# Kernel tuning notes

Hardware: AMD Instinct MI355X
Metric: run time of the kernel (lower is better)

The kernel has to match this reference:

```python
import jax, jax.numpy as jnp
import numpy as np


def _knn_idx(pts, k):
    # pts: [N, d] -> indices of k nearest neighbors (incl. self, loop=True) [N, k]
    sq = jnp.sum(pts * pts, axis=-1)
    d2 = sq[:, None] + sq[None, :] - 2.0 * (pts @ pts.T)  # [N, N] squared dists
    _, idx = jax.lax.top_k(-d2, k)  # k smallest distances
    return idx


def _graph_conv(x, nbr, Wr, br, Ws):
    # x: [B, N, d_in], nbr: [B, N, k]. GraphConv (aggr='add'):
    # out_i = W_rel @ sum_j x_j + b_rel + W_root @ x_i
    gathered = jax.vmap(lambda xb, ib: xb[ib])(x, nbr)  # [B, N, k, d_in]
    agg = gathered.sum(axis=2)                          # [B, N, d_in]
    return agg @ Wr.T + br + x @ Ws.T


def setup_inputs() -> dict:
    key = jax.random.key(0)
    ks = jax.random.split(key, 10)
    B, N, D, H = 16, 2048, 3, 128
    s = lambda fi, fo: (2.0 / (fi + fo)) ** 0.5
    return {
        "point_cloud": jax.random.normal(ks[0], (B, N, D), dtype=jnp.float32),
        "W1r": jax.random.normal(ks[1], (H, D), dtype=jnp.float32) * s(D, H),
        "b1": jnp.zeros((H,), dtype=jnp.float32),
        "W1s": jax.random.normal(ks[2], (H, D), dtype=jnp.float32) * s(D, H),
        "W2r": jax.random.normal(ks[3], (H, H), dtype=jnp.float32) * s(H, H),
        "b2": jnp.zeros((H,), dtype=jnp.float32),
        "W2s": jax.random.normal(ks[4], (H, H), dtype=jnp.float32) * s(H, H),
        "W3r": jax.random.normal(ks[5], (H, H), dtype=jnp.float32) * s(H, H),
        "b3": jnp.zeros((H,), dtype=jnp.float32),
        "W3s": jax.random.normal(ks[6], (H, H), dtype=jnp.float32) * s(H, H),
        "k": 16,
    }


def reference(point_cloud, W1r, b1, W1s, W2r, b2, W2s, W3r, b3, W3s, k):
    # knn graph per batch element (loop=True: self-loop included, d(i,i)=0)
    nbr = jax.vmap(lambda p: _knn_idx(p, k))(point_cloud)  # [B, N, k]
    x = jax.nn.relu(_graph_conv(point_cloud, nbr, W1r, b1, W1s))
    x = jax.nn.relu(_graph_conv(x, nbr, W2r, b2, W2s))
    x = _graph_conv(x, nbr, W3r, b3, W3s)
    return x  # [B, N, output_dim]
```

## Files before the change

### kernel.cpp

```cpp
#include <hip/hip_runtime.h>
#include <math.h>

#define NPTS 2048
#define BATCH 16
#define KNN 16
#define HID 128
#define RPB 8
#define CAP 128

typedef __attribute__((ext_vector_type(8))) short bf16x8;
typedef __attribute__((ext_vector_type(4))) float f32x4;

__device__ inline unsigned short f2bf(float f) {
    unsigned u = __float_as_uint(f);
    return (unsigned short)((u + 0x7FFFu + ((u >> 16) & 1u)) >> 16);
}
__device__ inline float bflo(unsigned v) { return __uint_as_float(v << 16); }
__device__ inline float bfhi(unsigned v) { return __uint_as_float(v & 0xFFFF0000u); }

__global__ __launch_bounds__(512) void knn_kernel(const float* __restrict__ pc,
                                                  int* __restrict__ nbr,
                                                  float4* __restrict__ aggpc)
{
    __shared__ __align__(16) float4 pts[NPTS];
    __shared__ unsigned ckey[RPB][CAP];
    __shared__ unsigned cidx[RPB][CAP];

    const int b = blockIdx.x >> 8;
    const int rblk = blockIdx.x & 255;
    const float* p = pc + (size_t)b * NPTS * 3;

    for (int t = threadIdx.x; t < NPTS; t += 512) {
        float x = p[t * 3 + 0], y = p[t * 3 + 1], z = p[t * 3 + 2];
        pts[t] = make_float4(x, y, z, x * x + y * y + z * z);
    }
    __syncthreads();

    const int w = threadIdx.x >> 6;
    const int lane = threadIdx.x & 63;
    const int i = rblk * RPB + w;
    const float4 pi = pts[i];

    unsigned key[32];
    #pragma unroll
    for (int t = 0; t < 32; ++t) {
        float4 c = pts[t * 64 + lane];
        float dot = fmaf(pi.x, c.x, fmaf(pi.y, c.y, pi.z * c.z));
        float d2 = fmaf(-2.0f, dot, pi.w + c.w);
        key[t] = __float_as_uint(d2 + 16.0f);
    }

    unsigned km = 0xFFFFFFFFu;
    #pragma unroll
    for (int t = 0; t < 32; ++t) km = min(km, key[t]);

    unsigned v = km;
    #pragma unroll
    for (int k = 2; k <= 64; k <<= 1) {
        #pragma unroll
        for (int j = k >> 1; j > 0; j >>= 1) {
            unsigned o = (unsigned)__shfl_xor((int)v, j, 64);
            bool up = ((lane & k) == 0);
            bool lower = ((lane & j) == 0);
            unsigned mn = min(v, o), mx = max(v, o);
            v = (up == lower) ? mn : mx;
        }
    }
    const unsigned T0 = (unsigned)__shfl((int)v, 15, 64);

    unsigned base = 0;
    #pragma unroll 1
    for (int t = 0; t < 32; ++t) {
        bool pred = key[t] <= T0;
        unsigned long long mask = __ballot(pred);
        if (mask) {
            unsigned prefix = __builtin_amdgcn_mbcnt_hi(
                (unsigned)(mask >> 32),
                __builtin_amdgcn_mbcnt_lo((unsigned)mask, 0));
            unsigned pos = base + prefix;
            if (pred && pos < CAP) {
                ckey[w][pos] = key[t];
                cidx[w][pos] = (unsigned)(t * 64 + lane);
            }
            base += (unsigned)__popcll(mask);
        }
    }
    __threadfence_block();
    const int m = (int)base;

    int* out = nbr + ((size_t)b * NPTS + i) * KNN;
    float ax = 0.f, ay = 0.f, az = 0.f;

    if (m <= CAP) {
        unsigned k0 = (lane < m) ? ckey[w][lane] : 0xFFFFFFFFu;
        unsigned k1 = (lane + 64 < m) ? ckey[w][lane + 64] : 0xFFFFFFFFu;
        int r0 = 0, r1 = 0;
        if (m <= 64) {
            #pragma unroll 1
            for (int jj = 0; jj < m; ++jj) {
                unsigned kj = ckey[w][jj];
                r0 += (kj < k0) || (kj == k0 && jj < lane);
            }
        } else {
            #pragma unroll 1
            for (int jj = 0; jj < m; ++jj) {
                unsigned kj = ckey[w][jj];
                r0 += (kj < k0) || (kj == k0 && jj < lane);
                r1 += (kj < k1) || (kj == k1 && jj < lane + 64);
            }
        }
        if (lane < m && r0 < KNN) {
            unsigned j = cidx[w][lane];
            out[r0] = (int)j;
            float4 q = pts[j]; ax += q.x; ay += q.y; az += q.z;
        }
        if (m > 64 && lane + 64 < m && r1 < KNN) {
            unsigned j = cidx[w][lane + 64];
            out[r1] = (int)j;
            float4 q = pts[j]; ax += q.x; ay += q.y; az += q.z;
        }
    } else {
        unsigned T = 0;
        #pragma unroll 1
        for (int bit = 31; bit >= 0; --bit) {
            unsigned trial = T | (1u << bit);
            int cnt = 0;
            #pragma unroll
            for (int t = 0; t < 32; ++t) cnt += (key[t] < trial);
            #pragma unroll
            for (int off = 32; off; off >>= 1)
                cnt += __shfl_xor(cnt, off, 64);
            if (cnt < KNN) T = trial;
        }
        unsigned bs = 0;
        #pragma unroll 1
        for (int t = 0; t < 32; ++t) {
            bool p1 = key[t] < T;
            unsigned long long mask = __ballot(p1);
            if (mask) {
                unsigned prefix = __builtin_amdgcn_mbcnt_hi(
                    (unsigned)(mask >> 32),
                    __builtin_amdgcn_mbcnt_lo((unsigned)mask, 0));
                if (p1) {
                    out[bs + prefix] = t * 64 + lane;
                    float4 q = pts[t * 64 + lane];
                    ax += q.x; ay += q.y; az += q.z;
                }
                bs += (unsigned)__popcll(mask);
            }
        }
        #pragma unroll 1
        for (int t = 0; t < 32 && bs < KNN; ++t) {
            bool p2 = key[t] == T;
            unsigned long long mask = __ballot(p2);
            if (mask) {
                unsigned prefix = __builtin_amdgcn_mbcnt_hi(
                    (unsigned)(mask >> 32),
                    __builtin_amdgcn_mbcnt_lo((unsigned)mask, 0));
                unsigned pos = bs + prefix;
                if (p2 && pos < KNN) {
                    out[pos] = t * 64 + lane;
                    float4 q = pts[t * 64 + lane];
                    ax += q.x; ay += q.y; az += q.z;
                }
                bs += (unsigned)__popcll(mask);
            }
        }
    }

    #pragma unroll
    for (int off = 32; off; off >>= 1) {
        ax += __shfl_xor(ax, off, 64);
        ay += __shfl_xor(ay, off, 64);
        az += __shfl_xor(az, off, 64);
    }
    if (lane == 0)
        aggpc[(size_t)b * NPTS + i] = make_float4(ax, ay, az, 0.f);
}

__global__ __launch_bounds__(256) void layer1_kernel(
    const float* __restrict__ pc, const float4* __restrict__ aggpc,
    const float* __restrict__ W1r, const float* __restrict__ b1,
    const float* __restrict__ W1s, unsigned short* __restrict__ x1)
{
    int gid = blockIdx.x * 256 + threadIdx.x;
    int p = gid >> 7;
    int h = gid & 127;
    float4 a = aggpc[p];
    float xx = pc[(size_t)p * 3 + 0];
    float xy = pc[(size_t)p * 3 + 1];
    float xz = pc[(size_t)p * 3 + 2];
    float acc = b1[h];
    acc += W1r[h * 3 + 0] * a.x + W1r[h * 3 + 1] * a.y + W1r[h * 3 + 2] * a.z;
    acc += W1s[h * 3 + 0] * xx + W1s[h * 3 + 1] * xy + W1s[h * 3 + 2] * xz;
    x1[gid] = f2bf(fmaxf(acc, 0.f));
}

__global__ __launch_bounds__(256) void wcvt_kernel(
    const float* __restrict__ a, const float* __restrict__ b,
    const float* __restrict__ c, const float* __restrict__ d,
    unsigned short* __restrict__ out)
{
    int g = blockIdx.x * 256 + threadIdx.x;
    int m = g >> 14;
    const float* s = (m == 0) ? a : (m == 1) ? b : (m == 2) ? c : d;
    out[g] = f2bf(s[g & 16383]);
}

template <bool RELU, bool OUT_BF16>
__global__ __launch_bounds__(512) void conv_fused(
    const unsigned short* __restrict__ x, const int* __restrict__ nbr,
    const unsigned short* __restrict__ Wr, const unsigned short* __restrict__ Ws,
    const float* __restrict__ bias, void* __restrict__ outv)
{
    __shared__ __align__(16) unsigned short aggs[64][136];
    __shared__ int nbrs[64][17];
    const int p0 = blockIdx.x * 64;
    const int bt = p0 >> 11;
    const unsigned short* xb = x + ((size_t)bt << 11) * HID;

    for (int e = threadIdx.x; e < 64 * KNN; e += 512)
        nbrs[e >> 4][e & 15] = nbr[(size_t)p0 * KNN + e];
    __syncthreads();

    #pragma unroll
    for (int it = 0; it < 2; ++it) {
        int task = it * 512 + threadIdx.x;
        int c8 = task & 15, pt = task >> 4;
        const unsigned short* base = xb + c8 * 8;
        float s[8] = {0, 0, 0, 0, 0, 0, 0, 0};
        #pragma unroll
        for (int t = 0; t < KNN; ++t) {
            int j = nbrs[pt][t];
            uint4 v = *(const uint4*)(base + (size_t)j * HID);
            s[0] += bflo(v.x); s[1] += bfhi(v.x);
            s[2] += bflo(v.y); s[3] += bfhi(v.y);
            s[4] += bflo(v.z); s[5] += bfhi(v.z);
            s[6] += bflo(v.w); s[7] += bfhi(v.w);
        }
        uint4 ov;
        ov.x = (unsigned)f2bf(s[0]) | ((unsigned)f2bf(s[1]) << 16);
        ov.y = (unsigned)f2bf(s[2]) | ((unsigned)f2bf(s[3]) << 16);
        ov.z = (unsigned)f2bf(s[4]) | ((unsigned)f2bf(s[5]) << 16);
        ov.w = (unsigned)f2bf(s[6]) | ((unsigned)f2bf(s[7]) << 16);
        *(uint4*)&aggs[pt][c8 * 8] = ov;
    }
    __syncthreads();

    const int wv = threadIdx.x >> 6;
    const int lane = threadIdx.x & 63;
    const int ptw = (wv & 1) * 32;
    const int h0w = (wv >> 1) * 32;
    const int row = lane & 15;
    const int quad = lane >> 4;

    f32x4 acc[2][2];
    #pragma unroll
    for (int i = 0; i < 2; ++i)
        #pragma unroll
        for (int n = 0; n < 2; ++n) acc[i][n] = (f32x4){0, 0, 0, 0};

    #pragma unroll
    for (int kc = 0; kc < 4; ++kc) {
        bf16x8 a0 = *(const bf16x8*)&aggs[ptw + row][quad * 8 + kc * 32];
        bf16x8 a1 = *(const bf16x8*)&aggs[ptw + 16 + row][quad * 8 + kc * 32];
        #pragma unroll
        for (int n = 0; n < 2; ++n) {
            bf16x8 bb = *(const bf16x8*)&Wr[(size_t)(h0w + n * 16 + row) * HID
                                            + quad * 8 + kc * 32];
            acc[0][n] = __builtin_amdgcn_mfma_f32_16x16x32_bf16(a0, bb, acc[0][n], 0, 0, 0);
            acc[1][n] = __builtin_amdgcn_mfma_f32_16x16x32_bf16(a1, bb, acc[1][n], 0, 0, 0);
        }
    }
    const unsigned short* xr0 = x + (size_t)(p0 + ptw + row) * HID + quad * 8;
    const unsigned short* xr1 = xr0 + 16 * HID;
    #pragma unroll
    for (int kc = 0; kc < 4; ++kc) {
        bf16x8 a0 = *(const bf16x8*)(xr0 + kc * 32);
        bf16x8 a1 = *(const bf16x8*)(xr1 + kc * 32);
        #pragma unroll
        for (int n = 0; n < 2; ++n) {
            bf16x8 bb = *(const bf16x8*)&Ws[(size_t)(h0w + n * 16 + row) * HID
                                            + quad * 8 + kc * 32];
            acc[0][n] = __builtin_amdgcn_mfma_f32_16x16x32_bf16(a0, bb, acc[0][n], 0, 0, 0);
            acc[1][n] = __builtin_amdgcn_mfma_f32_16x16x32_bf16(a1, bb, acc[1][n], 0, 0, 0);
        }
    }

    #pragma unroll
    for (int n = 0; n < 2; ++n) {
        float bh = bias[h0w + n * 16 + row];
        #pragma unroll
        for (int i = 0; i < 2; ++i) {
            #pragma unroll
            for (int r = 0; r < 4; ++r) {
                int pp = p0 + ptw + i * 16 + quad * 4 + r;
                float vv = acc[i][n][r] + bh;
                if (RELU) vv = fmaxf(vv, 0.f);
                if (OUT_BF16)
                    ((unsigned short*)outv)[(size_t)pp * HID + h0w + n * 16 + row] = f2bf(vv);
                else
                    ((float*)outv)[(size_t)pp * HID + h0w + n * 16 + row] = vv;
            }
        }
    }
}

extern "C" void kernel_launch(void* const* d_in, const int* in_sizes, int n_in,
                              void* d_out, int out_size, void* d_ws, size_t ws_size,
                              hipStream_t stream)
{
    const float* pc  = (const float*)d_in[0];
    const float* W1r = (const float*)d_in[1];
    const float* b1  = (const float*)d_in[2];
    const float* W1s = (const float*)d_in[3];
    const float* W2r = (const float*)d_in[4];
    const float* b2  = (const float*)d_in[5];
    const float* W2s = (const float*)d_in[6];
    const float* W3r = (const float*)d_in[7];
    const float* b3  = (const float*)d_in[8];
    const float* W3s = (const float*)d_in[9];
    float* out = (float*)d_out;

    char* ws = (char*)d_ws;
    const size_t MB = 1024 * 1024;
    int*            nbr   = (int*)ws;
    float4*         aggpc = (float4*)(ws + 2 * MB);
    unsigned short* x1    = (unsigned short*)(ws + 3 * MB);
    unsigned short* x2    = (unsigned short*)(ws + 3 * MB + 8388608);
    unsigned short* wbf   = (unsigned short*)(ws + 3 * MB + 2 * 8388608);
    unsigned short* w2r = wbf;
    unsigned short* w2s = wbf + 16384;
    unsigned short* w3r = wbf + 32768;
    unsigned short* w3s = wbf + 49152;

    const int NPOINTS = BATCH * NPTS;

    knn_kernel<<<NPOINTS / RPB, 512, 0, stream>>>(pc, nbr, aggpc);
    layer1_kernel<<<NPOINTS * HID / 256, 256, 0, stream>>>(
        pc, aggpc, W1r, b1, W1s, x1);
    wcvt_kernel<<<256, 256, 0, stream>>>(W2r, W2s, W3r, W3s, wbf);

    conv_fused<true, true><<<NPOINTS / 64, 512, 0, stream>>>(
        x1, nbr, w2r, w2s, b2, x2);
    conv_fused<false, false><<<NPOINTS / 64, 512, 0, stream>>>(
        x2, nbr, w3r, w3s, b3, out);
}
```

Measured before the change: 184.7 us.

## Fuse layer-1 GraphConv into KNN kernel and use LDS atomics for candidate compaction

Folds the first GraphConv layer into the KNN kernel, so each wavefront writes its bf16 128-wide output row directly and the aggpc buffer and a separate kernel launch go away. Candidate collection switches from ballot/mbcnt prefix compaction to per-wave LDS atomicAdd, storing key and index together as uint2. Ties are now broken by index rather than by slot position, since atomic ordering is nondeterministic. The wcvt launch moves ahead of KNN. The trade-offs are possible LDS atomic contention and a heavier KNN epilogue.

```diff
diff --git a/kernel.cpp b/kernel.cpp
--- a/kernel.cpp
+++ b/kernel.cpp
@@ -18,13 +18,14 @@
 __device__ inline float bflo(unsigned v) { return __uint_as_float(v << 16); }
 __device__ inline float bfhi(unsigned v) { return __uint_as_float(v & 0xFFFF0000u); }
 
-__global__ __launch_bounds__(512) void knn_kernel(const float* __restrict__ pc,
-                                                  int* __restrict__ nbr,
-                                                  float4* __restrict__ aggpc)
+__global__ __launch_bounds__(512) void knn_kernel(
+    const float* __restrict__ pc, int* __restrict__ nbr,
+    const float* __restrict__ W1r, const float* __restrict__ b1,
+    const float* __restrict__ W1s, unsigned short* __restrict__ x1)
 {
     __shared__ __align__(16) float4 pts[NPTS];
-    __shared__ unsigned ckey[RPB][CAP];
-    __shared__ unsigned cidx[RPB][CAP];
+    __shared__ uint2 cand[RPB][CAP];
+    __shared__ unsigned ccnt[RPB];
 
     const int b = blockIdx.x >> 8;
     const int rblk = blockIdx.x & 255;
@@ -40,19 +41,21 @@
     const int lane = threadIdx.x & 63;
     const int i = rblk * RPB + w;
     const float4 pi = pts[i];
+    const float piw16 = pi.w + 16.0f;
+
+    if (lane == 0) ccnt[w] = 0;
+    __threadfence_block();
 
     unsigned key[32];
+    unsigned km = 0xFFFFFFFFu;
     #pragma unroll
     for (int t = 0; t < 32; ++t) {
         float4 c = pts[t * 64 + lane];
         float dot = fmaf(pi.x, c.x, fmaf(pi.y, c.y, pi.z * c.z));
-        float d2 = fmaf(-2.0f, dot, pi.w + c.w);
-        key[t] = __float_as_uint(d2 + 16.0f);
-    }
-
-    unsigned km = 0xFFFFFFFFu;
-    #pragma unroll
-    for (int t = 0; t < 32; ++t) km = min(km, key[t]);
+        float d2 = fmaf(-2.0f, dot, piw16 + c.w);
+        key[t] = __float_as_uint(d2);
+        km = min(km, key[t]);
+    }
 
     unsigned v = km;
     #pragma unroll
@@ -60,64 +63,53 @@
         #pragma unroll
         for (int j = k >> 1; j > 0; j >>= 1) {
             unsigned o = (unsigned)__shfl_xor((int)v, j, 64);
-            bool up = ((lane & k) == 0);
-            bool lower = ((lane & j) == 0);
-            unsigned mn = min(v, o), mx = max(v, o);
-            v = (up == lower) ? mn : mx;
+            bool sel = ((lane & k) == 0) == ((lane & j) == 0);
+            v = sel ? min(v, o) : max(v, o);
         }
     }
     const unsigned T0 = (unsigned)__shfl((int)v, 15, 64);
 
-    unsigned base = 0;
     #pragma unroll 1
     for (int t = 0; t < 32; ++t) {
-        bool pred = key[t] <= T0;
-        unsigned long long mask = __ballot(pred);
-        if (mask) {
-            unsigned prefix = __builtin_amdgcn_mbcnt_hi(
-                (unsigned)(mask >> 32),
-                __builtin_amdgcn_mbcnt_lo((unsigned)mask, 0));
-            unsigned pos = base + prefix;
-            if (pred && pos < CAP) {
-                ckey[w][pos] = key[t];
-                cidx[w][pos] = (unsigned)(t * 64 + lane);
-            }
-            base += (unsigned)__popcll(mask);
+        if (key[t] <= T0) {
+            unsigned pos = atomicAdd(&ccnt[w], 1u);
+            if (pos < CAP)
+                cand[w][pos] = make_uint2(key[t], (unsigned)(t * 64 + lane));
         }
     }
     __threadfence_block();
-    const int m = (int)base;
+    const int m = (int)ccnt[w];
 
     int* out = nbr + ((size_t)b * NPTS + i) * KNN;
     float ax = 0.f, ay = 0.f, az = 0.f;
 
     if (m <= CAP) {
-        unsigned k0 = (lane < m) ? ckey[w][lane] : 0xFFFFFFFFu;
-        unsigned k1 = (lane + 64 < m) ? ckey[w][lane + 64] : 0xFFFFFFFFu;
-        int r0 = 0, r1 = 0;
+        uint2 e0 = (lane < m) ? cand[w][lane] : make_uint2(0xFFFFFFFFu, 0xFFFFFFFFu);
+        int r0 = 0;
         if (m <= 64) {
             #pragma unroll 1
             for (int jj = 0; jj < m; ++jj) {
-                unsigned kj = ckey[w][jj];
-                r0 += (kj < k0) || (kj == k0 && jj < lane);
+                uint2 cj = cand[w][jj];
+                r0 += (cj.x < e0.x) || (cj.x == e0.x && cj.y < e0.y);
             }
         } else {
+            uint2 e1 = (lane + 64 < m) ? cand[w][lane + 64]
+                                       : make_uint2(0xFFFFFFFFu, 0xFFFFFFFFu);
+            int r1 = 0;
             #pragma unroll 1
             for (int jj = 0; jj < m; ++jj) {
-                unsigned kj = ckey[w][jj];
-                r0 += (kj < k0) || (kj == k0 && jj < lane);
-                r1 += (kj < k1) || (kj == k1 && jj < lane + 64);
+                uint2 cj = cand[w][jj];
+                r0 += (cj.x < e0.x) || (cj.x == e0.x && cj.y < e0.y);
+                r1 += (cj.x < e1.x) || (cj.x == e1.x && cj.y < e1.y);
+            }
+            if (lane + 64 < m && r1 < KNN) {
+                out[r1] = (int)e1.y;
+                float4 q = pts[e1.y]; ax += q.x; ay += q.y; az += q.z;
             }
         }
         if (lane < m && r0 < KNN) {
-            unsigned j = cidx[w][lane];
-            out[r0] = (int)j;
-            float4 q = pts[j]; ax += q.x; ay += q.y; az += q.z;
-        }
-        if (m > 64 && lane + 64 < m && r1 < KNN) {
-            unsigned j = cidx[w][lane + 64];
-            out[r1] = (int)j;
-            float4 q = pts[j]; ax += q.x; ay += q.y; az += q.z;
+            out[r0] = (int)e0.y;
+            float4 q = pts[e0.y]; ax += q.x; ay += q.y; az += q.z;
         }
     } else {
         unsigned T = 0;
@@ -174,26 +166,16 @@
         ay += __shfl_xor(ay, off, 64);
         az += __shfl_xor(az, off, 64);
     }
-    if (lane == 0)
-        aggpc[(size_t)b * NPTS + i] = make_float4(ax, ay, az, 0.f);
-}
-
-__global__ __launch_bounds__(256) void layer1_kernel(
-    const float* __restrict__ pc, const float4* __restrict__ aggpc,
-    const float* __restrict__ W1r, const float* __restrict__ b1,
-    const float* __restrict__ W1s, unsigned short* __restrict__ x1)
-{
-    int gid = blockIdx.x * 256 + threadIdx.x;
-    int p = gid >> 7;
-    int h = gid & 127;
-    float4 a = aggpc[p];
-    float xx = pc[(size_t)p * 3 + 0];
-    float xy = pc[(size_t)p * 3 + 1];
-    float xz = pc[(size_t)p * 3 + 2];
-    float acc = b1[h];
-    acc += W1r[h * 3 + 0] * a.x + W1r[h * 3 + 1] * a.y + W1r[h * 3 + 2] * a.z;
-    acc += W1s[h * 3 + 0] * xx + W1s[h * 3 + 1] * xy + W1s[h * 3 + 2] * xz;
-    x1[gid] = f2bf(fmaxf(acc, 0.f));
+
+    unsigned short* xrow = x1 + ((size_t)b * NPTS + i) * HID;
+    #pragma unroll
+    for (int hh = 0; hh < 2; ++hh) {
+        int h = lane + hh * 64;
+        float acc = b1[h];
+        acc += W1r[h * 3 + 0] * ax + W1r[h * 3 + 1] * ay + W1r[h * 3 + 2] * az;
+        acc += W1s[h * 3 + 0] * pi.x + W1s[h * 3 + 1] * pi.y + W1s[h * 3 + 2] * pi.z;
+        xrow[h] = f2bf(fmaxf(acc, 0.f));
+    }
 }
 
 __global__ __launch_bounds__(256) void wcvt_kernel(
@@ -324,11 +306,10 @@
 
     char* ws = (char*)d_ws;
     const size_t MB = 1024 * 1024;
-    int*            nbr   = (int*)ws;
-    float4*         aggpc = (float4*)(ws + 2 * MB);
-    unsigned short* x1    = (unsigned short*)(ws + 3 * MB);
-    unsigned short* x2    = (unsigned short*)(ws + 3 * MB + 8388608);
-    unsigned short* wbf   = (unsigned short*)(ws + 3 * MB + 2 * 8388608);
+    int*            nbr = (int*)ws;
+    unsigned short* x1  = (unsigned short*)(ws + 2 * MB);
+    unsigned short* x2  = (unsigned short*)(ws + 2 * MB + 8388608);
+    unsigned short* wbf = (unsigned short*)(ws + 2 * MB + 2 * 8388608);
     unsigned short* w2r = wbf;
     unsigned short* w2s = wbf + 16384;
     unsigned short* w3r = wbf + 32768;
@@ -336,10 +317,8 @@
 
     const int NPOINTS = BATCH * NPTS;
 
-    knn_kernel<<<NPOINTS / RPB, 512, 0, stream>>>(pc, nbr, aggpc);
-    layer1_kernel<<<NPOINTS * HID / 256, 256, 0, stream>>>(
-        pc, aggpc, W1r, b1, W1s, x1);
     wcvt_kernel<<<256, 256, 0, stream>>>(W2r, W2s, W3r, W3s, wbf);
+    knn_kernel<<<NPOINTS / RPB, 512, 0, stream>>>(pc, nbr, W1r, b1, W1s, x1);
 
     conv_fused<true, true><<<NPOINTS / 64, 512, 0, stream>>>(
         x1, nbr, w2r, w2s, b2, x2);
```

New measurement: 196.8 us. +6.6%, slower.

## Fuse layer-1 conv into kNN epilogue and widen conv blocks to 1024 threads

Applied to the files above, without the earlier changes.

The first GraphConv layer is computed directly in the kNN kernel's epilogue from the wave-reduced neighbor sum. This removes the separate layer1 launch and the aggpc intermediate buffer. The fused conv kernel now uses 1024 threads, with one gather task per thread and 16x32 MFMA tiles per wave instead of 32x32, for more parallelism in the gather phase. The kNN distance loop also folds the bias constant and the min reduction into one pass. The stricter launch bound may limit registers and reduce per-wave reuse of weight loads.

```diff
diff --git a/kernel.cpp b/kernel.cpp
--- a/kernel.cpp
+++ b/kernel.cpp
@@ -18,9 +18,10 @@
 __device__ inline float bflo(unsigned v) { return __uint_as_float(v << 16); }
 __device__ inline float bfhi(unsigned v) { return __uint_as_float(v & 0xFFFF0000u); }
 
-__global__ __launch_bounds__(512) void knn_kernel(const float* __restrict__ pc,
-                                                  int* __restrict__ nbr,
-                                                  float4* __restrict__ aggpc)
+__global__ __launch_bounds__(512) void knn_kernel(
+    const float* __restrict__ pc, int* __restrict__ nbr,
+    const float* __restrict__ W1r, const float* __restrict__ b1,
+    const float* __restrict__ W1s, unsigned short* __restrict__ x1)
 {
     __shared__ __align__(16) float4 pts[NPTS];
     __shared__ unsigned ckey[RPB][CAP];
@@ -40,19 +41,18 @@
     const int lane = threadIdx.x & 63;
     const int i = rblk * RPB + w;
     const float4 pi = pts[i];
+    const float piw16 = pi.w + 16.0f;
 
     unsigned key[32];
+    unsigned km = 0xFFFFFFFFu;
     #pragma unroll
     for (int t = 0; t < 32; ++t) {
         float4 c = pts[t * 64 + lane];
         float dot = fmaf(pi.x, c.x, fmaf(pi.y, c.y, pi.z * c.z));
-        float d2 = fmaf(-2.0f, dot, pi.w + c.w);
-        key[t] = __float_as_uint(d2 + 16.0f);
-    }
-
-    unsigned km = 0xFFFFFFFFu;
-    #pragma unroll
-    for (int t = 0; t < 32; ++t) km = min(km, key[t]);
+        float d2 = fmaf(-2.0f, dot, piw16 + c.w);
+        key[t] = __float_as_uint(d2);
+        km = min(km, key[t]);
+    }
 
     unsigned v = km;
     #pragma unroll
@@ -60,10 +60,8 @@
         #pragma unroll
         for (int j = k >> 1; j > 0; j >>= 1) {
             unsigned o = (unsigned)__shfl_xor((int)v, j, 64);
-            bool up = ((lane & k) == 0);
-            bool lower = ((lane & j) == 0);
-            unsigned mn = min(v, o), mx = max(v, o);
-            v = (up == lower) ? mn : mx;
+            bool sel = ((lane & k) == 0) == ((lane & j) == 0);
+            v = sel ? min(v, o) : max(v, o);
         }
     }
     const unsigned T0 = (unsigned)__shfl((int)v, 15, 64);
@@ -174,26 +172,16 @@
         ay += __shfl_xor(ay, off, 64);
         az += __shfl_xor(az, off, 64);
     }
-    if (lane == 0)
-        aggpc[(size_t)b * NPTS + i] = make_float4(ax, ay, az, 0.f);
-}
-
-__global__ __launch_bounds__(256) void layer1_kernel(
-    const float* __restrict__ pc, const float4* __restrict__ aggpc,
-    const float* __restrict__ W1r, const float* __restrict__ b1,
-    const float* __restrict__ W1s, unsigned short* __restrict__ x1)
-{
-    int gid = blockIdx.x * 256 + threadIdx.x;
-    int p = gid >> 7;
-    int h = gid & 127;
-    float4 a = aggpc[p];
-    float xx = pc[(size_t)p * 3 + 0];
-    float xy = pc[(size_t)p * 3 + 1];
-    float xz = pc[(size_t)p * 3 + 2];
-    float acc = b1[h];
-    acc += W1r[h * 3 + 0] * a.x + W1r[h * 3 + 1] * a.y + W1r[h * 3 + 2] * a.z;
-    acc += W1s[h * 3 + 0] * xx + W1s[h * 3 + 1] * xy + W1s[h * 3 + 2] * xz;
-    x1[gid] = f2bf(fmaxf(acc, 0.f));
+
+    unsigned short* xrow = x1 + ((size_t)b * NPTS + i) * HID;
+    #pragma unroll
+    for (int hh = 0; hh < 2; ++hh) {
+        int h = lane + hh * 64;
+        float acc = b1[h];
+        acc += W1r[h * 3 + 0] * ax + W1r[h * 3 + 1] * ay + W1r[h * 3 + 2] * az;
+        acc += W1s[h * 3 + 0] * pi.x + W1s[h * 3 + 1] * pi.y + W1s[h * 3 + 2] * pi.z;
+        xrow[h] = f2bf(fmaxf(acc, 0.f));
+    }
 }
 
 __global__ __launch_bounds__(256) void wcvt_kernel(
@@ -208,7 +196,7 @@
 }
 
 template <bool RELU, bool OUT_BF16>
-__global__ __launch_bounds__(512) void conv_fused(
+__global__ __launch_bounds__(1024, 8) void conv_fused(
     const unsigned short* __restrict__ x, const int* __restrict__ nbr,
     const unsigned short* __restrict__ Wr, const unsigned short* __restrict__ Ws,
     const float* __restrict__ bias, void* __restrict__ outv)
@@ -219,14 +207,14 @@
     const int bt = p0 >> 11;
     const unsigned short* xb = x + ((size_t)bt << 11) * HID;
 
-    for (int e = threadIdx.x; e < 64 * KNN; e += 512)
+    {
+        int e = threadIdx.x;
         nbrs[e >> 4][e & 15] = nbr[(size_t)p0 * KNN + e];
+    }
     __syncthreads();
 
-    #pragma unroll
-    for (int it = 0; it < 2; ++it) {
-        int task = it * 512 + threadIdx.x;
-        int c8 = task & 15, pt = task >> 4;
+    {
+        int c8 = threadIdx.x & 15, pt = threadIdx.x >> 4;
         const unsigned short* base = xb + c8 * 8;
         float s[8] = {0, 0, 0, 0, 0, 0, 0, 0};
         #pragma unroll
@@ -249,41 +237,34 @@
 
     const int wv = threadIdx.x >> 6;
     const int lane = threadIdx.x & 63;
-    const int ptw = (wv & 1) * 32;
-    const int h0w = (wv >> 1) * 32;
+    const int ptw = (wv & 3) * 16;
+    const int h0w = (wv >> 2) * 32;
     const int row = lane & 15;
     const int quad = lane >> 4;
 
-    f32x4 acc[2][2];
-    #pragma unroll
-    for (int i = 0; i < 2; ++i)
-        #pragma unroll
-        for (int n = 0; n < 2; ++n) acc[i][n] = (f32x4){0, 0, 0, 0};
+    f32x4 acc[2];
+    acc[0] = (f32x4){0, 0, 0, 0};
+    acc[1] = (f32x4){0, 0, 0, 0};
 
     #pragma unroll
     for (int kc = 0; kc < 4; ++kc) {
         bf16x8 a0 = *(const bf16x8*)&aggs[ptw + row][quad * 8 + kc * 32];
-        bf16x8 a1 = *(const bf16x8*)&aggs[ptw + 16 + row][quad * 8 + kc * 32];
         #pragma unroll
         for (int n = 0; n < 2; ++n) {
             bf16x8 bb = *(const bf16x8*)&Wr[(size_t)(h0w + n * 16 + row) * HID
                                             + quad * 8 + kc * 32];
-            acc[0][n] = __builtin_amdgcn_mfma_f32_16x16x32_bf16(a0, bb, acc[0][n], 0, 0, 0);
-            acc[1][n] = __builtin_amdgcn_mfma_f32_16x16x32_bf16(a1, bb, acc[1][n], 0, 0, 0);
+            acc[n] = __builtin_amdgcn_mfma_f32_16x16x32_bf16(a0, bb, acc[n], 0, 0, 0);
         }
     }
     const unsigned short* xr0 = x + (size_t)(p0 + ptw + row) * HID + quad * 8;
-    const unsigned short* xr1 = xr0 + 16 * HID;
     #pragma unroll
     for (int kc = 0; kc < 4; ++kc) {
         bf16x8 a0 = *(const bf16x8*)(xr0 + kc * 32);
-        bf16x8 a1 = *(const bf16x8*)(xr1 + kc * 32);
         #pragma unroll
         for (int n = 0; n < 2; ++n) {
             bf16x8 bb = *(const bf16x8*)&Ws[(size_t)(h0w + n * 16 + row) * HID
                                             + quad * 8 + kc * 32];
-            acc[0][n] = __builtin_amdgcn_mfma_f32_16x16x32_bf16(a0, bb, acc[0][n], 0, 0, 0);
-            acc[1][n] = __builtin_amdgcn_mfma_f32_16x16x32_bf16(a1, bb, acc[1][n], 0, 0, 0);
+            acc[n] = __builtin_amdgcn_mfma_f32_16x16x32_bf16(a0, bb, acc[n], 0, 0, 0);
         }
     }
 
@@ -291,17 +272,14 @@
     for (int n = 0; n < 2; ++n) {
         float bh = bias[h0w + n * 16 + row];
         #pragma unroll
-        for (int i = 0; i < 2; ++i) {
-            #pragma unroll
-            for (int r = 0; r < 4; ++r) {
-                int pp = p0 + ptw + i * 16 + quad * 4 + r;
-                float vv = acc[i][n][r] + bh;
-                if (RELU) vv = fmaxf(vv, 0.f);
-                if (OUT_BF16)
-                    ((unsigned short*)outv)[(size_t)pp * HID + h0w + n * 16 + row] = f2bf(vv);
-                else
-                    ((float*)outv)[(size_t)pp * HID + h0w + n * 16 + row] = vv;
-            }
+        for (int r = 0; r < 4; ++r) {
+            int pp = p0 + ptw + quad * 4 + r;
+            float vv = acc[n][r] + bh;
+            if (RELU) vv = fmaxf(vv, 0.f);
+            if (OUT_BF16)
+                ((unsigned short*)outv)[(size_t)pp * HID + h0w + n * 16 + row] = f2bf(vv);
+            else
+                ((float*)outv)[(size_t)pp * HID + h0w + n * 16 + row] = vv;
         }
     }
 }
@@ -324,11 +302,10 @@
 
     char* ws = (char*)d_ws;
     const size_t MB = 1024 * 1024;
-    int*            nbr   = (int*)ws;
-    float4*         aggpc = (float4*)(ws + 2 * MB);
-    unsigned short* x1    = (unsigned short*)(ws + 3 * MB);
-    unsigned short* x2    = (unsigned short*)(ws + 3 * MB + 8388608);
-    unsigned short* wbf   = (unsigned short*)(ws + 3 * MB + 2 * 8388608);
+    int*            nbr = (int*)ws;
+    unsigned short* x1  = (unsigned short*)(ws + 2 * MB);
+    unsigned short* x2  = (unsigned short*)(ws + 2 * MB + 8388608);
+    unsigned short* wbf = (unsigned short*)(ws + 2 * MB + 2 * 8388608);
     unsigned short* w2r = wbf;
     unsigned short* w2s = wbf + 16384;
     unsigned short* w3r = wbf + 32768;
@@ -336,13 +313,11 @@
 
     const int NPOINTS = BATCH * NPTS;
 
-    knn_kernel<<<NPOINTS / RPB, 512, 0, stream>>>(pc, nbr, aggpc);
-    layer1_kernel<<<NPOINTS * HID / 256, 256, 0, stream>>>(
-        pc, aggpc, W1r, b1, W1s, x1);
     wcvt_kernel<<<256, 256, 0, stream>>>(W2r, W2s, W3r, W3s, wbf);
-
-    conv_fused<true, true><<<NPOINTS / 64, 512, 0, stream>>>(
+    knn_kernel<<<NPOINTS / RPB, 512, 0, stream>>>(pc, nbr, W1r, b1, W1s, x1);
+
+    conv_fused<true, true><<<NPOINTS / 64, 1024, 0, stream>>>(
         x1, nbr, w2r, w2s, b2, x2);
-    conv_fused<false, false><<<NPOINTS / 64, 512, 0, stream>>>(
+    conv_fused<false, false><<<NPOINTS / 64, 1024, 0, stream>>>(
         x2, nbr, w3r, w3s, b3, out);
 }
```

Measured after the change: 185.1 us. About the same (+0.2%).
